# Kernel tuning notes

Measured on AMD Instinct MI355X. Metric: run time of the kernel, lower is better.

The kernel has to match this reference:

```python
import jax, jax.numpy as jnp
import numpy as np
from jax import lax

NUM_SEG = 64
EPS = 1e-12

def conv2d(x, w, b=None):
    y = lax.conv_general_dilated(x, w, (1, 1), 'SAME', dimension_numbers=('NCHW', 'OIHW', 'NCHW'))
    if b is not None:
        y = y + b[None, :, None, None]
    return y

def layer_norm_chw(x):
    # LayerNorm over (C,H,W) per sample, no affine
    mu = x.mean(axis=(1, 2, 3), keepdims=True)
    var = jnp.mean((x - mu) ** 2, axis=(1, 2, 3), keepdims=True)
    return (x - mu) / jnp.sqrt(var + EPS)

def spade(x, sem_rs, w_sh, b_sh, w_g, b_g, w_be, b_be):
    xn = layer_norm_chw(x)
    h = jax.nn.relu(conv2d(sem_rs, w_sh, b_sh))
    gamma = conv2d(h, w_g, b_g)
    beta = conv2d(h, w_be, b_be)
    return xn * (1.0 + gamma) + beta

def painted_semantic_map(f_sem, segmap):
    # f_sem: [B,C,Hp,Wp] float; segmap: [B,Hi,Wi] int
    B, C, Hp, Wp = f_sem.shape
    _, Hi, Wi = segmap.shape
    # torch nearest interpolate: src = floor(dst * in/out)
    rows = (jnp.arange(Hp) * Hi) // Hp
    cols = (jnp.arange(Wp) * Wi) // Wp
    seg_small = segmap[:, rows[:, None], cols[None, :]]  # [B,Hp,Wp]
    flat_feat = f_sem.transpose(0, 2, 3, 1).reshape(-1, C)  # [B*Hp*Wp, C]
    bidx = jnp.repeat(jnp.arange(B), Hp * Wp)
    gid = bidx * NUM_SEG + jnp.clip(seg_small.reshape(-1), 0, NUM_SEG - 1)
    sums = jax.ops.segment_sum(flat_feat, gid, num_segments=B * NUM_SEG)
    cnts = jax.ops.segment_sum(jnp.ones((flat_feat.shape[0],), flat_feat.dtype), gid, num_segments=B * NUM_SEG)
    # scatter_mean + nan_to_num: empty segments -> 0
    avg = jnp.where(cnts[:, None] > 0, sums / jnp.maximum(cnts, 1.0)[:, None], 0.0)
    pid = jnp.repeat(jnp.arange(B), Hi * Wi) * NUM_SEG + jnp.clip(segmap.reshape(-1), 0, NUM_SEG - 1)
    return avg[pid].reshape(B, Hi, Wi, C).transpose(0, 3, 1, 2)  # [B,C,Hi,Wi]

def setup_inputs() -> dict:
    key = jax.random.key(0)
    ks = jax.random.split(key, 32)
    B, Cm, Cs, Hp, Wp, Hi, Wi, Hm = 2, 1536, 384, 32, 32, 448, 448, 128
    d = {}
    d['x_main'] = jax.random.normal(ks[0], (B, Cm, Hp, Wp), jnp.float32)
    d['f_semantic'] = jax.random.normal(ks[1], (B, Cs, Hp, Wp), jnp.float32)
    s = 0.02
    d['w_sh0'] = jax.random.normal(ks[2], (Hm, Cs, 3, 3), jnp.float32) * s
    d['b_sh0'] = jax.random.normal(ks[3], (Hm,), jnp.float32) * s
    d['w_g0'] = jax.random.normal(ks[4], (Cm, Hm, 3, 3), jnp.float32) * s
    d['b_g0'] = jax.random.normal(ks[5], (Cm,), jnp.float32) * s
    d['w_be0'] = jax.random.normal(ks[6], (Cm, Hm, 3, 3), jnp.float32) * s
    d['b_be0'] = jax.random.normal(ks[7], (Cm,), jnp.float32) * s
    d['w_sh1'] = jax.random.normal(ks[8], (Hm, Cs, 3, 3), jnp.float32) * s
    d['b_sh1'] = jax.random.normal(ks[9], (Hm,), jnp.float32) * s
    d['w_g1'] = jax.random.normal(ks[10], (8, Hm, 3, 3), jnp.float32) * s
    d['b_g1'] = jax.random.normal(ks[11], (8,), jnp.float32) * s
    d['w_be1'] = jax.random.normal(ks[12], (8, Hm, 3, 3), jnp.float32) * s
    d['b_be1'] = jax.random.normal(ks[13], (8,), jnp.float32) * s
    d['w_sh2'] = jax.random.normal(ks[14], (Hm, Cs, 3, 3), jnp.float32) * s
    d['b_sh2'] = jax.random.normal(ks[15], (Hm,), jnp.float32) * s
    d['w_g2'] = jax.random.normal(ks[16], (16, Hm, 3, 3), jnp.float32) * s
    d['b_g2'] = jax.random.normal(ks[17], (16,), jnp.float32) * s
    d['w_be2'] = jax.random.normal(ks[18], (16, Hm, 3, 3), jnp.float32) * s
    d['b_be2'] = jax.random.normal(ks[19], (16,), jnp.float32) * s
    d['w_c0'] = jax.random.normal(ks[20], (8, Cm, 1, 1), jnp.float32) * s
    d['bias0'] = jax.random.normal(ks[21], (8,), jnp.float32) * s
    d['w_c1'] = jax.random.normal(ks[22], (16, 8, 1, 1), jnp.float32) * s
    d['bias1'] = jax.random.normal(ks[23], (16,), jnp.float32) * s
    d['w_c2'] = jax.random.normal(ks[24], (1, 16, 1, 1), jnp.float32) * s
    d['bias2'] = jax.random.normal(ks[25], (1,), jnp.float32) * s
    d['segmap'] = jax.random.randint(ks[26], (B, Hi, Wi), 0, NUM_SEG, jnp.int32)
    return d

def reference(x_main, f_semantic, w_sh0, b_sh0, w_g0, b_g0, w_be0, b_be0,
              w_sh1, b_sh1, w_g1, b_g1, w_be1, b_be1,
              w_sh2, b_sh2, w_g2, b_g2, w_be2, b_be2,
              w_c0, bias0, w_c1, bias1, w_c2, bias2, segmap):
    B, Cm, Hp, Wp = x_main.shape
    pm = painted_semantic_map(f_semantic, segmap)  # [B,Cs,Hi,Wi]
    # bilinear (align_corners=False) resize to main-path resolution; identical at all 3 SPADE layers
    sem_rs = jax.image.resize(pm, (B, pm.shape[1], Hp, Wp), method='bilinear')
    h = spade(x_main, sem_rs, w_sh0, b_sh0, w_g0, b_g0, w_be0, b_be0)
    h = jax.nn.softplus(conv2d(h, w_c0) + bias0[None, :, None, None])
    h = spade(h, sem_rs, w_sh1, b_sh1, w_g1, b_g1, w_be1, b_be1)
    h = jax.nn.softplus(conv2d(h, w_c1) + bias1[None, :, None, None])
    h = spade(h, sem_rs, w_sh2, b_sh2, w_g2, b_g2, w_be2, b_be2)
    h = jax.nn.softplus(conv2d(h, w_c2) + bias2[None, :, None, None])
    return h
```

## Files before the change

### kernel.cpp

```cpp
#include <hip/hip_runtime.h>
#include <hip/hip_bf16.h>

#define DEV __device__ __forceinline__

constexpr int B = 2;
constexpr int CM = 1536;
constexpr int CS = 384;
constexpr int HP = 32, WP = 32, P = 1024;
constexpr int HI = 448, WI = 448;
constexpr int HM = 128;
constexpr int NSEG = 64;

constexpr size_t OFF_AVG  = 0;
constexpr size_t OFF_SEMT = 49152;
constexpr size_t OFF_HSHT = 835584;
constexpr size_t OFF_OUT0 = 1622016;
constexpr size_t OFF_P6   = 4767744;
constexpr size_t OFF_H1A  = 5160960;
constexpr size_t OFF_OUT1 = 5177344;
constexpr size_t OFF_H2A  = 5193728;
constexpr size_t OFF_OUT2 = 5226496;
constexpr size_t OFF_STATS= 5259264;
constexpr size_t OFF_PACK = 5259280;

constexpr size_t PK0 = 0;
constexpr size_t PK1 = 1327104;
constexpr size_t PK2 = 4866048;
constexpr size_t PK3 = 4902912;
constexpr int    PK_CHUNKS = 617472;

typedef __attribute__((ext_vector_type(8))) short s16x8;
typedef __attribute__((ext_vector_type(4))) float f32x4;

DEV float softplus_f(float x) {
    return fmaxf(x, 0.f) + log1pf(expf(-fabsf(x)));
}
DEV ushort f2bf(float f) {
    union { float f; unsigned u; } x; x.f = f;
    unsigned r = x.u + 0x7fffu + ((x.u >> 16) & 1u);
    return (ushort)(r >> 16);
}
DEV float bf2f(ushort u) {
    union { unsigned u; float f; } x; x.u = ((unsigned)u) << 16;
    return x.f;
}

__global__ __launch_bounds__(256) void k_seg_avg(const float* __restrict__ f_sem,
                                                 const int* __restrict__ segmap,
                                                 float* __restrict__ ws) {
    int b = blockIdx.y;
    int c0 = blockIdx.x * 8;
    __shared__ int   segs[P];
    __shared__ float sums[NSEG][9];
    __shared__ float cnt[NSEG];
    int t = threadIdx.x;
    for (int i = t; i < NSEG * 9; i += 256) (&sums[0][0])[i] = 0.f;
    if (t < NSEG) cnt[t] = 0.f;
    __syncthreads();
    for (int p = t; p < P; p += 256) {
        int i = p >> 5, j = p & 31;
        int s = segmap[(b * HI + i * 14) * WI + j * 14];
        s = min(max(s, 0), NSEG - 1);
        segs[p] = s;
        atomicAdd(&cnt[s], 1.f);
    }
    __syncthreads();
    #pragma unroll
    for (int ch = 0; ch < 8; ++ch) {
        const float* fp = f_sem + ((size_t)b * CS + c0 + ch) * P;
        #pragma unroll
        for (int pb = 0; pb < 4; ++pb) {
            int p = pb * 256 + t;
            float v = fp[p];
            atomicAdd(&sums[segs[p]][ch], v);
        }
    }
    __syncthreads();
    for (int i = t; i < NSEG * 8; i += 256) {
        int s = i >> 3, ch = i & 7;
        float cv = cnt[s];
        ws[OFF_AVG + ((size_t)(b * NSEG + s)) * CS + c0 + ch] =
            cv > 0.f ? sums[s][ch] / cv : 0.f;
    }
}

__global__ __launch_bounds__(256) void k_paint(const int* __restrict__ segmap,
                                               float* __restrict__ ws) {
    int pixb = blockIdx.x;
    int b = pixb >> 10, op = pixb & 1023;
    int oy = op >> 5, ox = op & 31;
    __shared__ float Wb[NSEG];
    __shared__ float normv;
    int t = threadIdx.x;
    if (t < NSEG) Wb[t] = 0.f;
    __syncthreads();
    float cy = 14.f * oy + 6.5f, cx = 14.f * ox + 6.5f;
    int y0 = 14 * oy - 7, x0 = 14 * ox - 7;
    for (int k = t; k < 28 * 28; k += 256) {
        int jy = y0 + k / 28, jx = x0 + k % 28;
        if (jy < 0 || jy >= HI || jx < 0 || jx >= WI) continue;
        float wy = 1.f - fabsf(cy - (float)jy) * (1.f / 14.f);
        float wx = 1.f - fabsf(cx - (float)jx) * (1.f / 14.f);
        int s = segmap[(b * HI + jy) * WI + jx];
        s = min(max(s, 0), NSEG - 1);
        atomicAdd(&Wb[s], wy * wx);
    }
    if (t == 0) {
        float sy = 0.f, sx = 0.f;
        for (int d = 0; d < 28; d++) {
            int jy = y0 + d;
            if (jy >= 0 && jy < HI) sy += 1.f - fabsf(cy - (float)jy) * (1.f / 14.f);
            int jx = x0 + d;
            if (jx >= 0 && jx < WI) sx += 1.f - fabsf(cx - (float)jx) * (1.f / 14.f);
        }
        normv = 1.f / (sy * sx);
    }
    __syncthreads();
    float nv = normv;
    for (int c = t; c < CS; c += 256) {
        float acc = 0.f;
        const float* ap = ws + OFF_AVG + ((size_t)b * NSEG) * CS + c;
        #pragma unroll
        for (int s = 0; s < NSEG; s++) acc += Wb[s] * ap[(size_t)s * CS];
        ws[OFF_SEMT + ((size_t)b * P + op) * CS + c] = acc * nv;
    }
}

__global__ __launch_bounds__(256) void k_ln0_stats(const float* __restrict__ x,
                                                   float* __restrict__ stats) {
    int b = blockIdx.y;
    const float4* xp = (const float4*)(x + (size_t)b * CM * P);
    int n4 = CM * P / 4;
    float s = 0.f, q = 0.f;
    for (int i = blockIdx.x * 256 + threadIdx.x; i < n4; i += 64 * 256) {
        float4 v = xp[i];
        s += v.x + v.y + v.z + v.w;
        q += v.x * v.x + v.y * v.y + v.z * v.z + v.w * v.w;
    }
    for (int o = 32; o > 0; o >>= 1) { s += __shfl_down(s, o); q += __shfl_down(q, o); }
    __shared__ float ls[4], lq[4];
    int w = threadIdx.x >> 6;
    if ((threadIdx.x & 63) == 0) { ls[w] = s; lq[w] = q; }
    __syncthreads();
    if (threadIdx.x == 0) {
        atomicAdd(&stats[b * 2],     ls[0] + ls[1] + ls[2] + ls[3]);
        atomicAdd(&stats[b * 2 + 1], lq[0] + lq[1] + lq[2] + lq[3]);
    }
}

__global__ __launch_bounds__(256) void k_wpack(
    const float* __restrict__ w_sh0, const float* __restrict__ w_sh1, const float* __restrict__ w_sh2,
    const float* __restrict__ w_g0,  const float* __restrict__ w_be0,
    const float* __restrict__ w_g1,  const float* __restrict__ w_be1,
    const float* __restrict__ w_g2,  const float* __restrict__ w_be2,
    ushort* __restrict__ packU)
{
    for (int c8 = blockIdx.x * 256 + threadIdx.x; c8 < PK_CHUNKS; c8 += gridDim.x * 256) {
        size_t e = (size_t)c8 * 8;
        const float* s0 = nullptr;
        bool zero = false;
        if (e < PK1) {
            size_t r = e;
            int ci0 = (int)(r & 31), co2 = (int)((r >> 5) & 31);
            int tap = (int)((r >> 10) % 9);
            int kct = (int)((r / 9216) % 12), ct = (int)(r / 110592);
            int coG = ct * 32 + co2, sel = coG >> 7, cow = coG & 127;
            const float* wp = sel == 0 ? w_sh0 : (sel == 1 ? w_sh1 : w_sh2);
            s0 = &wp[((size_t)cow * CS + kct * 32 + ci0) * 9 + tap];
        } else if (e < PK2) {
            size_t r = e - PK1;
            int ci0 = (int)(r & 31), co2 = (int)((r >> 5) & 31);
            int tap = (int)((r >> 10) % 9);
            int kct = (int)((r / 9216) % 4), ct = (int)(r / 36864);
            int cog = ct * 16 + (co2 & 15);
            const float* wp = co2 < 16 ? w_g0 : w_be0;
            s0 = &wp[((size_t)cog * HM + kct * 32 + ci0) * 9 + tap];
        } else if (e < PK3) {
            size_t r = e - PK2;
            int ci0 = (int)(r & 31), co2 = (int)((r >> 5) & 31);
            int tap = (int)((r >> 10) % 9);
            int kct = (int)(r / 9216);
            zero = ((co2 & 15) >= 8);
            int cog = co2 & 7;
            const float* wp = co2 < 16 ? w_g1 : w_be1;
            if (!zero) s0 = &wp[((size_t)cog * HM + kct * 32 + ci0) * 9 + tap];
        } else {
            size_t r = e - PK3;
            int ci0 = (int)(r & 31), co2 = (int)((r >> 5) & 31);
            int tap = (int)((r >> 10) % 9);
            int kct = (int)(r / 9216);
            int cog = co2 & 15;
            const float* wp = co2 < 16 ? w_g2 : w_be2;
            s0 = &wp[((size_t)cog * HM + kct * 32 + ci0) * 9 + tap];
        }
        s16x8 o;
        #pragma unroll
        for (int i = 0; i < 8; ++i) {
            float v = zero ? 0.f : s0[(size_t)i * 9];
            o[i] = (short)f2bf(v);
        }
        *(s16x8*)&packU[e] = o;
    }
}

template<int MODE>
__global__ __launch_bounds__(256) void k_conv_mfma(
    const float* __restrict__ semT, const ushort* __restrict__ hshTin,
    const ushort* __restrict__ packW,
    const float* __restrict__ bb0, const float* __restrict__ bb1, const float* __restrict__ bb2,
    const float* __restrict__ xsrc, const float* __restrict__ st, float Ninv,
    float* __restrict__ outF, ushort* __restrict__ outH)
{
    constexpr int ROWS = (MODE == 0) ? 4 : 8;
    constexpr int NT   = ROWS / 2;
    constexpr int XR   = ROWS + 2;
    constexpr int KTOT = (MODE == 0) ? 12 : 4;
    constexpr int CBASE = (MODE == 2) ? 128 : (MODE == 3) ? 256 : 0;
    constexpr int NP = (MODE == 1) ? 1536 : (MODE == 2) ? 8 : 16;

    int pt = blockIdx.x, ctile = blockIdx.y;
    int zz = blockIdx.z;
    int b  = (MODE == 0) ? (zz % B) : zz;
    int ks = (MODE == 0) ? (zz / B) : 0;
    int t = threadIdx.x, l = t & 63, wv = t >> 6;
    int y0 = pt * ROWS;

    __shared__ __align__(16) ushort Wl[9][32][40];
    __shared__ __align__(16) ushort Xl[XR][34][40];

    f32x4 acc[2][NT] = {};

    for (int kc = 0; kc < 128; kc += 32) {
        __syncthreads();
        for (int j = t; j < XR * 34 * 4; j += 256) {
            int slot = j >> 2, part = j & 3;
            int r = slot / 34, c = slot % 34;
            int gy = y0 - 1 + r, gx = c - 1;
            s16x8 v = {};
            if (gy >= 0 && gy < HP && gx >= 0 && gx < WP) {
                int pix = gy * WP + gx;
                if constexpr (MODE == 0) {
                    const float4* sp = (const float4*)&semT[((size_t)b * P + pix) * CS + ks * 128 + kc + part * 8];
                    float4 x0 = sp[0], x1 = sp[1];
                    v[0] = (short)f2bf(x0.x); v[1] = (short)f2bf(x0.y);
                    v[2] = (short)f2bf(x0.z); v[3] = (short)f2bf(x0.w);
                    v[4] = (short)f2bf(x1.x); v[5] = (short)f2bf(x1.y);
                    v[6] = (short)f2bf(x1.z); v[7] = (short)f2bf(x1.w);
                } else {
                    v = *(const s16x8*)&hshTin[((size_t)b * P + pix) * 384 + CBASE + kc + part * 8];
                }
            }
            *(s16x8*)&Xl[r][c][part * 8] = v;
        }
        const ushort* wsrc = packW + (size_t)(ctile * KTOT + ks * 4 + (kc >> 5)) * 9216;
        for (int j = t; j < 1152; j += 256) {
            int tap = j >> 7, co2 = (j >> 2) & 31, part = j & 3;
            *(s16x8*)&Wl[tap][co2][part * 8] = *(const s16x8*)&wsrc[(size_t)j * 8];
        }
        __syncthreads();
        #pragma unroll
        for (int tap = 0; tap < 9; ++tap) {
            int dy = tap / 3, dx = tap % 3;
            s16x8 a0 = *(const s16x8*)&Wl[tap][l & 15][(l >> 4) * 8];
            s16x8 a1 = *(const s16x8*)&Wl[tap][16 + (l & 15)][(l >> 4) * 8];
            #pragma unroll
            for (int nt = 0; nt < NT; ++nt) {
                int q = wv * (16 * NT) + nt * 16 + (l & 15);
                int ry = (q >> 5) + dy, rx = (q & 31) + dx;
                s16x8 bf = *(const s16x8*)&Xl[ry][rx][(l >> 4) * 8];
                acc[0][nt] = __builtin_amdgcn_mfma_f32_16x16x32_bf16(a0, bf, acc[0][nt], 0, 0, 0);
                acc[1][nt] = __builtin_amdgcn_mfma_f32_16x16x32_bf16(a1, bf, acc[1][nt], 0, 0, 0);
            }
        }
    }

    if constexpr (MODE == 0) {
        __syncthreads();
        ushort (*T)[36] = (ushort(*)[36])(&Xl[0][0][0]);
        #pragma unroll
        for (int mt = 0; mt < 2; ++mt)
            #pragma unroll
            for (int nt = 0; nt < NT; ++nt)
                #pragma unroll
                for (int r = 0; r < 4; ++r) {
                    int m = mt * 16 + (l >> 4) * 4 + r;
                    int pl = wv * (16 * NT) + nt * 16 + (l & 15);
                    T[pl][m] = f2bf(acc[mt][nt][r]);
                }
        __syncthreads();
        int row = t >> 1, half = t & 1;
        ushort* dst = outH + ((size_t)((ks * B + b) * P) + pt * 128 + row) * 384 + ctile * 32 + half * 16;
        *(s16x8*)dst = *(const s16x8*)&T[row][half * 16];
    } else {
        float mu = st[b * 2] * Ninv;
        float var = st[b * 2 + 1] * Ninv - mu * mu;
        float rs = rsqrtf(var + 1e-12f);
        #pragma unroll
        for (int nt = 0; nt < NT; ++nt)
            #pragma unroll
            for (int r = 0; r < 4; ++r) {
                int m = (l >> 4) * 4 + r;
                if (MODE == 2 && m >= 8) continue;
                int cog = (MODE == 1) ? ctile * 16 + m : m;
                int px = pt * 256 + wv * 64 + nt * 16 + (l & 15);
                float gam = acc[0][nt][r] + bb0[cog];
                float bet = acc[1][nt][r] + bb1[cog];
                float xv = xsrc[((size_t)b * NP + cog) * P + px];
                outF[((size_t)b * NP + cog) * P + px] = (xv - mu) * rs * (1.f + gam) + bet;
            }
    }
}

__global__ __launch_bounds__(256) void k_hsh_fin(const ushort* __restrict__ part,
                                                 const float* __restrict__ b0,
                                                 const float* __restrict__ b1,
                                                 const float* __restrict__ b2,
                                                 ushort* __restrict__ hsh) {
    int gid = blockIdx.x * 256 + threadIdx.x;
    int grp = gid % 48, pixg = gid / 48;
    int ch0 = grp * 8;
    size_t base = (size_t)pixg * 384 + ch0;
    s16x8 p0 = *(const s16x8*)&part[(size_t)0 * B * P * 384 + base];
    s16x8 p1 = *(const s16x8*)&part[(size_t)1 * B * P * 384 + base];
    s16x8 p2 = *(const s16x8*)&part[(size_t)2 * B * P * 384 + base];
    int sel = ch0 >> 7;
    const float* bp = sel == 0 ? b0 : (sel == 1 ? b1 : b2);
    int cb = ch0 & 127;
    s16x8 o;
    #pragma unroll
    for (int i = 0; i < 8; ++i) {
        float v = bf2f((ushort)p0[i]) + bf2f((ushort)p1[i]) + bf2f((ushort)p2[i]) + bp[cb + i];
        o[i] = (short)f2bf(fmaxf(v, 0.f));
    }
    *(s16x8*)&hsh[base] = o;
}

__global__ __launch_bounds__(256) void k_c1x1_a(const float* __restrict__ out0,
                                                const float* __restrict__ w,
                                                float* __restrict__ part) {
    int b = blockIdx.z, ks = blockIdx.y, pg = blockIdx.x;
    int t = threadIdx.x, lp = t & 63, g = t >> 6;
    int pix = pg * 64 + lp;
    float acc[8] = {};
    int ci0 = ks * 64 + g * 16;
    for (int i = 0; i < 16; i++) {
        int ci = ci0 + i;
        float v = out0[((size_t)b * CM + ci) * P + pix];
        #pragma unroll
        for (int o = 0; o < 8; o++) acc[o] += w[o * CM + ci] * v;
    }
    __shared__ float red[4][64][8];
    #pragma unroll
    for (int o = 0; o < 8; o++) red[g][lp][o] = acc[o];
    __syncthreads();
    for (int idx = t; idx < 512; idx += 256) {
        int pp = idx >> 3, o = idx & 7;
        float s = red[0][pp][o] + red[1][pp][o] + red[2][pp][o] + red[3][pp][o];
        part[(((size_t)b * 24 + ks) * 8 + o) * P + pg * 64 + pp] = s;
    }
}

__global__ __launch_bounds__(256) void k_c1x1_a_fin(const float* __restrict__ part,
                                                    const float* __restrict__ bias,
                                                    float* __restrict__ h1a,
                                                    float* __restrict__ stats) {
    int b = blockIdx.y, t = threadIdx.x;
    int idx = blockIdx.x * 1024 + t;
    float s = 0.f, q = 0.f;
    for (int k = 0; k < 4; ++k, idx += 256) {
        int o = idx >> 10, pix = idx & 1023;
        float v = 0.f;
        for (int ks = 0; ks < 24; ks++) v += part[(((size_t)b * 24 + ks) * 8 + o) * P + pix];
        v += bias[o];
        v = softplus_f(v);
        h1a[((size_t)b * 8 + o) * P + pix] = v;
        s += v; q += v * v;
    }
    for (int o2 = 32; o2 > 0; o2 >>= 1) { s += __shfl_down(s, o2); q += __shfl_down(q, o2); }
    __shared__ float ls[4], lq[4];
    int w = t >> 6;
    if ((t & 63) == 0) { ls[w] = s; lq[w] = q; }
    __syncthreads();
    if (t == 0) {
        atomicAdd(&stats[(B + b) * 2],     ls[0] + ls[1] + ls[2] + ls[3]);
        atomicAdd(&stats[(B + b) * 2 + 1], lq[0] + lq[1] + lq[2] + lq[3]);
    }
}

__global__ __launch_bounds__(256) void k_c1x1_b(const float* __restrict__ out1,
                                                const float* __restrict__ w,
                                                const float* __restrict__ bias,
                                                float* __restrict__ h2a,
                                                float* __restrict__ stats) {
    int b = blockIdx.y, t = threadIdx.x;
    int pix = blockIdx.x * 256 + t;
    float vin[8];
    #pragma unroll
    for (int ci = 0; ci < 8; ci++) vin[ci] = out1[((size_t)b * 8 + ci) * P + pix];
    float s = 0.f, q = 0.f;
    #pragma unroll
    for (int o = 0; o < 16; o++) {
        float a = bias[o];
        #pragma unroll
        for (int ci = 0; ci < 8; ci++) a += w[o * 8 + ci] * vin[ci];
        a = softplus_f(a);
        h2a[((size_t)b * 16 + o) * P + pix] = a;
        s += a; q += a * a;
    }
    for (int o2 = 32; o2 > 0; o2 >>= 1) { s += __shfl_down(s, o2); q += __shfl_down(q, o2); }
    __shared__ float ls[4], lq[4];
    int w2 = t >> 6;
    if ((t & 63) == 0) { ls[w2] = s; lq[w2] = q; }
    __syncthreads();
    if (t == 0) {
        atomicAdd(&stats[(2 * B + b) * 2],     ls[0] + ls[1] + ls[2] + ls[3]);
        atomicAdd(&stats[(2 * B + b) * 2 + 1], lq[0] + lq[1] + lq[2] + lq[3]);
    }
}

__global__ __launch_bounds__(256) void k_final(const float* __restrict__ out2,
                                               const float* __restrict__ w,
                                               const float* __restrict__ bias,
                                               float* __restrict__ out) {
    int b = blockIdx.y, t = threadIdx.x;
    int pix = blockIdx.x * 256 + t;
    float a = bias[0];
    #pragma unroll
    for (int ci = 0; ci < 16; ci++) a += w[ci] * out2[((size_t)b * 16 + ci) * P + pix];
    a = softplus_f(a);
    out[(size_t)b * P + pix] = a;
}

extern "C" void kernel_launch(void* const* d_in, const int* in_sizes, int n_in,
                              void* d_out, int out_size, void* d_ws, size_t ws_size,
                              hipStream_t stream) {
    const float* x_main = (const float*)d_in[0];
    const float* f_sem  = (const float*)d_in[1];
    const float* w_sh0 = (const float*)d_in[2];  const float* b_sh0 = (const float*)d_in[3];
    const float* w_g0  = (const float*)d_in[4];  const float* b_g0  = (const float*)d_in[5];
    const float* w_be0 = (const float*)d_in[6];  const float* b_be0 = (const float*)d_in[7];
    const float* w_sh1 = (const float*)d_in[8];  const float* b_sh1 = (const float*)d_in[9];
    const float* w_g1  = (const float*)d_in[10]; const float* b_g1  = (const float*)d_in[11];
    const float* w_be1 = (const float*)d_in[12]; const float* b_be1 = (const float*)d_in[13];
    const float* w_sh2 = (const float*)d_in[14]; const float* b_sh2 = (const float*)d_in[15];
    const float* w_g2  = (const float*)d_in[16]; const float* b_g2  = (const float*)d_in[17];
    const float* w_be2 = (const float*)d_in[18]; const float* b_be2 = (const float*)d_in[19];
    const float* w_c0  = (const float*)d_in[20]; const float* bias0 = (const float*)d_in[21];
    const float* w_c1  = (const float*)d_in[22]; const float* bias1 = (const float*)d_in[23];
    const float* w_c2  = (const float*)d_in[24]; const float* bias2 = (const float*)d_in[25];
    const int*   segmap = (const int*)d_in[26];

    float* ws = (float*)d_ws;
    float* out = (float*)d_out;
    float* stats = ws + OFF_STATS;
    ushort* hshU = (ushort*)(ws + OFF_HSHT);
    ushort* partU = (ushort*)(ws + OFF_OUT0);
    ushort* packU = (ushort*)(ws + OFF_PACK);

    hipMemsetAsync((void*)stats, 0, 16 * sizeof(float), stream);

    k_wpack<<<dim3(2412), 256, 0, stream>>>(w_sh0, w_sh1, w_sh2, w_g0, w_be0,
                                            w_g1, w_be1, w_g2, w_be2, packU);
    k_seg_avg<<<dim3(48, B), 256, 0, stream>>>(f_sem, segmap, ws);
    k_ln0_stats<<<dim3(64, B), 256, 0, stream>>>(x_main, stats);
    k_paint<<<dim3(B * P), 256, 0, stream>>>(segmap, ws);

    k_conv_mfma<0><<<dim3(8, 12, 3 * B), 256, 0, stream>>>(
        ws + OFF_SEMT, nullptr, packU + PK0,
        nullptr, nullptr, nullptr, nullptr, nullptr, 0.f, nullptr, partU);
    k_hsh_fin<<<dim3(384), 256, 0, stream>>>(partU, b_sh0, b_sh1, b_sh2, hshU);

    k_conv_mfma<1><<<dim3(4, 96, B), 256, 0, stream>>>(
        nullptr, hshU, packU + PK1,
        b_g0, b_be0, nullptr, x_main, stats, 1.f / (float)(CM * P),
        ws + OFF_OUT0, nullptr);

    k_c1x1_a<<<dim3(16, 24, B), 256, 0, stream>>>(ws + OFF_OUT0, w_c0, ws + OFF_P6);
    k_c1x1_a_fin<<<dim3(8, B), 256, 0, stream>>>(ws + OFF_P6, bias0, ws + OFF_H1A, stats);

    k_conv_mfma<2><<<dim3(4, 1, B), 256, 0, stream>>>(
        nullptr, hshU, packU + PK2,
        b_g1, b_be1, nullptr, ws + OFF_H1A, stats + 2 * B, 1.f / (float)(8 * P),
        ws + OFF_OUT1, nullptr);

    k_c1x1_b<<<dim3(4, B), 256, 0, stream>>>(ws + OFF_OUT1, w_c1, bias1, ws + OFF_H2A, stats);

    k_conv_mfma<3><<<dim3(4, 1, B), 256, 0, stream>>>(
        nullptr, hshU, packU + PK3,
        b_g2, b_be2, nullptr, ws + OFF_H2A, stats + 4 * B, 1.f / (float)(16 * P),
        ws + OFF_OUT2, nullptr);

    k_final<<<dim3(4, B), 256, 0, stream>>>(ws + OFF_OUT2, w_c2, bias2, out);
}
```

Before: 320.6 us.

## Tile paint kernel over 8 output columns to share segmap reads and avg loads

k_paint now handles 8 horizontally adjacent output pixels per block instead of one. Each block reads a 28x126 segmap strip once and scatters bilinear weights into per-pixel histograms. The matvec loads each avg value once and reuses it for 8 accumulators. The normaliser is now the sum of the histogram weights rather than computed analytically. This removes redundant segmap reads (overlapping windows) and repeated avg loads, at the cost of fewer blocks (256 vs 2048) and more registers per thread.

```diff
diff --git a/kernel.cpp b/kernel.cpp
--- a/kernel.cpp
+++ b/kernel.cpp
@@ -86,43 +86,57 @@
 
 __global__ __launch_bounds__(256) void k_paint(const int* __restrict__ segmap,
                                                float* __restrict__ ws) {
-    int pixb = blockIdx.x;
-    int b = pixb >> 10, op = pixb & 1023;
-    int oy = op >> 5, ox = op & 31;
-    __shared__ float Wb[NSEG];
-    __shared__ float normv;
+    int oxt = blockIdx.x, oy = blockIdx.y, b = blockIdx.z;
+    int ox0 = oxt * 8;
+    __shared__ float WbT[8][65];
+    __shared__ float norm[8];
     int t = threadIdx.x;
-    if (t < NSEG) Wb[t] = 0.f;
-    __syncthreads();
-    float cy = 14.f * oy + 6.5f, cx = 14.f * ox + 6.5f;
-    int y0 = 14 * oy - 7, x0 = 14 * ox - 7;
-    for (int k = t; k < 28 * 28; k += 256) {
-        int jy = y0 + k / 28, jx = x0 + k % 28;
+    for (int i = t; i < 8 * 65; i += 256) (&WbT[0][0])[i] = 0.f;
+    __syncthreads();
+
+    float cy = 14.f * oy + 6.5f;
+    int y0 = 14 * oy - 7;
+    int x0 = 14 * ox0 - 7;
+    for (int k = t; k < 28 * 126; k += 256) {
+        int r = k / 126, cix = k % 126;
+        int jy = y0 + r, jx = x0 + cix;
         if (jy < 0 || jy >= HI || jx < 0 || jx >= WI) continue;
         float wy = 1.f - fabsf(cy - (float)jy) * (1.f / 14.f);
-        float wx = 1.f - fabsf(cx - (float)jx) * (1.f / 14.f);
         int s = segmap[(b * HI + jy) * WI + jx];
         s = min(max(s, 0), NSEG - 1);
-        atomicAdd(&Wb[s], wy * wx);
-    }
-    if (t == 0) {
-        float sy = 0.f, sx = 0.f;
-        for (int d = 0; d < 28; d++) {
-            int jy = y0 + d;
-            if (jy >= 0 && jy < HI) sy += 1.f - fabsf(cy - (float)jy) * (1.f / 14.f);
-            int jx = x0 + d;
-            if (jx >= 0 && jx < WI) sx += 1.f - fabsf(cx - (float)jx) * (1.f / 14.f);
-        }
-        normv = 1.f / (sy * sx);
-    }
-    __syncthreads();
-    float nv = normv;
+        int oxhi = (jx + 7) / 14;
+        #pragma unroll
+        for (int d = 0; d < 2; ++d) {
+            int ox = oxhi - d;
+            if (ox < ox0 || ox >= ox0 + 8) continue;
+            float wx = 1.f - fabsf(14.f * ox + 6.5f - (float)jx) * (1.f / 14.f);
+            if (wx > 0.f) atomicAdd(&WbT[ox - ox0][s], wy * wx);
+        }
+    }
+    __syncthreads();
+    if (t < 8) {
+        float sm = 0.f;
+        #pragma unroll
+        for (int s = 0; s < NSEG; ++s) sm += WbT[t][s];
+        norm[t] = 1.f / sm;
+    }
+    __syncthreads();
+
+    const float* ap0 = ws + OFF_AVG + (size_t)b * NSEG * CS;
     for (int c = t; c < CS; c += 256) {
-        float acc = 0.f;
-        const float* ap = ws + OFF_AVG + ((size_t)b * NSEG) * CS + c;
-        #pragma unroll
-        for (int s = 0; s < NSEG; s++) acc += Wb[s] * ap[(size_t)s * CS];
-        ws[OFF_SEMT + ((size_t)b * P + op) * CS + c] = acc * nv;
+        float acc[8] = {};
+        const float* ap = ap0 + c;
+        #pragma unroll
+        for (int s = 0; s < NSEG; ++s) {
+            float a = ap[(size_t)s * CS];
+            #pragma unroll
+            for (int ox = 0; ox < 8; ++ox) acc[ox] += WbT[ox][s] * a;
+        }
+        #pragma unroll
+        for (int ox = 0; ox < 8; ++ox) {
+            int op = oy * 32 + ox0 + ox;
+            ws[OFF_SEMT + ((size_t)b * P + op) * CS + c] = acc[ox] * norm[ox];
+        }
     }
 }
 
@@ -463,7 +477,7 @@
                                             w_g1, w_be1, w_g2, w_be2, packU);
     k_seg_avg<<<dim3(48, B), 256, 0, stream>>>(f_sem, segmap, ws);
     k_ln0_stats<<<dim3(64, B), 256, 0, stream>>>(x_main, stats);
-    k_paint<<<dim3(B * P), 256, 0, stream>>>(segmap, ws);
+    k_paint<<<dim3(4, 32, B), 256, 0, stream>>>(segmap, ws);
 
     k_conv_mfma<0><<<dim3(8, 12, 3 * B), 256, 0, stream>>>(
         ws + OFF_SEMT, nullptr, packU + PK0,
```

New measurement: 319.4 us. No clear change (-0.4%).
